# Optimization experiments

Hardware: AMD Instinct MI355X
Metric: run time of the kernel (lower is better)

## Reference

```python
import jax, jax.numpy as jnp
import numpy as np

N_NODES = 100000
N_EDGES = 1600000
N_FEAT = 128
N_HID = 128
N_CLASS = 10
N_GRAPHS = 512
BN_EPS = 1e-5


def setup_inputs() -> dict:
    key = jax.random.key(0)
    ks = jax.random.split(key, 12)
    x = jax.random.normal(ks[0], (N_NODES, N_FEAT), dtype=jnp.float32)
    edge_index = jax.random.randint(ks[1], (2, N_EDGES), 0, N_NODES, dtype=jnp.int32)
    batch = jnp.sort(jax.random.randint(ks[2], (N_NODES,), 0, N_GRAPHS, dtype=jnp.int32))
    s1 = 1.0 / np.sqrt(N_FEAT)
    s2 = 1.0 / np.sqrt(N_HID)
    W1 = jax.random.uniform(ks[3], (N_FEAT, N_HID), jnp.float32, -s1, s1)
    b1 = jax.random.uniform(ks[4], (N_HID,), jnp.float32, -s1, s1)
    gamma = jnp.ones((N_HID,), jnp.float32)
    beta = jnp.zeros((N_HID,), jnp.float32)
    W2 = jax.random.uniform(ks[5], (N_HID, N_HID), jnp.float32, -s2, s2)
    b2 = jax.random.uniform(ks[6], (N_HID,), jnp.float32, -s2, s2)
    clsW = jax.random.uniform(ks[7], (N_HID, N_CLASS), jnp.float32, -s2, s2)
    clsb = jax.random.uniform(ks[8], (N_CLASS,), jnp.float32, -s2, s2)
    return {"x": x, "edge_index": edge_index, "batch": batch,
            "W1": W1, "b1": b1, "gamma": gamma, "beta": beta,
            "W2": W2, "b2": b2, "clsW": clsW, "clsb": clsb}


def _gcn_norm(edge_index, n_nodes):
    # add self-loops, compute symmetric normalization D^-1/2 A_hat D^-1/2
    loops = jnp.arange(n_nodes, dtype=edge_index.dtype)
    src = jnp.concatenate([edge_index[0], loops])
    dst = jnp.concatenate([edge_index[1], loops])
    deg = jax.ops.segment_sum(jnp.ones_like(dst, dtype=jnp.float32), dst,
                              num_segments=n_nodes)
    dinv = jnp.where(deg > 0, jax.lax.rsqrt(deg), 0.0)
    norm = dinv[src] * dinv[dst]  # [E + N]
    return src, dst, norm


def _gcn_conv(h, src, dst, norm, W, b, n_nodes):
    h = h @ W                                   # [N, nhid] dense GEMM
    msg = h[src] * norm[:, None]                # gather + scale  [E+N, nhid]
    out = jax.ops.segment_sum(msg, dst, num_segments=n_nodes)  # scatter-add
    return out + b


def reference(x, edge_index, batch, W1, b1, gamma, beta, W2, b2, clsW, clsb):
    n_nodes = x.shape[0]
    src, dst, norm = _gcn_norm(edge_index, n_nodes)
    # layer 1: GCNConv -> BatchNorm(eval, running stats 0/1) -> ReLU -> Dropout(eval=id)
    h = _gcn_conv(x, src, dst, norm, W1, b1, n_nodes)
    h = h * (gamma / jnp.sqrt(1.0 + BN_EPS)) + beta
    h = jax.nn.relu(h)
    # layer 2: GCNConv (output layer, no bn/act)
    h = _gcn_conv(h, src, dst, norm, W2, b2, n_nodes)
    # global mean pool over batch index
    sums = jax.ops.segment_sum(h, batch, num_segments=N_GRAPHS)          # [G, nhid]
    cnts = jax.ops.segment_sum(jnp.ones((n_nodes,), h.dtype), batch,
                               num_segments=N_GRAPHS)
    g = sums / jnp.maximum(cnts, 1.0)[:, None]
    out = jax.nn.log_softmax(g @ clsW + clsb, axis=1)                    # [G, nclass]
    return out, g
```

## Files before the change

### kernel.cpp

```cpp
#include <hip/hip_runtime.h>
#include <hip/hip_bf16.h>

#define N_NODES 100000
#define N_EDGES 1600000
#define N_FEAT 128
#define N_HID 128
#define N_CLASS 10
#define N_GRAPHS 512
#define BN_RSQRT 0.9999950000374997f

#define NRANGE 12500
#define NSUB 512
#define SCAP 640
#define HGROUP 32
#define BPB (NSUB / HGROUP)

#define XT_STRIDE 136
#define YW_STRIDE 36
#define FG_LDS 78848

typedef _Float16 half_t;
typedef __attribute__((ext_vector_type(2))) _Float16 half2v;
typedef __attribute__((ext_vector_type(4))) _Float16 half4v;
typedef __attribute__((ext_vector_type(8))) _Float16 half8v;
typedef __attribute__((ext_vector_type(4))) float floatx4;
typedef __attribute__((ext_vector_type(2))) float floatx2;

__global__ __launch_bounds__(256) void bucket_fused(
    const int* __restrict__ src, const int* __restrict__ dst,
    int* __restrict__ cnt, unsigned long long* __restrict__ bucketed,
    const float* __restrict__ W1, half_t* __restrict__ Wt1,
    const float* __restrict__ W2, half_t* __restrict__ Wt2,
    const int* __restrict__ batch, int* __restrict__ boffs,
    int* __restrict__ sentinel,
    int chunkE, int E, int nnodes)
{
    __shared__ int wcnt[4][8];
    __shared__ int wbase[4][8];
    int blk = blockIdx.x;
    if (blk >= NSUB) {
        int k = blk - NSUB;
        if (k == 0) {
            if (threadIdx.x < 32) sentinel[threadIdx.x] = 0;
        } else if (k <= 128) {
            int i = (k - 1) * 256 + threadIdx.x;
            const float* W = (i < 16384) ? W1 : W2;
            half_t* Wt = (i < 16384) ? Wt1 : Wt2;
            int j = i & 16383;
            int c = j >> 7, kk = j & 127;
            Wt[(size_t)c * 128 + kk] = (half_t)W[(size_t)kk * 128 + c];
        } else {
            int i = (k - 129) * 256 + threadIdx.x;
            if (i < nnodes) {
                int b = batch[i];
                int prev = (i == 0) ? -1 : batch[i - 1];
                for (int g = prev + 1; g <= b; ++g) boffs[g] = i;
                if (i == nnodes - 1)
                    for (int g = b + 1; g <= N_GRAPHS; ++g) boffs[g] = nnodes;
            }
        }
        return;
    }
    int b = blk;
    int wave = threadIdx.x >> 6;
    int lane = threadIdx.x & 63;
    int e0 = b * chunkE;
    int e1 = e0 + chunkE < E ? e0 + chunkE : E;
    int iters = (chunkE + 255) / 256;

    int mycnt = 0;
    for (int it = 0; it < iters; ++it) {
        int e = e0 + it * 256 + threadIdx.x;
        bool valid = e < e1;
        int d = valid ? dst[e] : 0;
        int rr = (d * 8) / N_NODES;
#pragma unroll
        for (int r = 0; r < 8; ++r) {
            unsigned long long m = __ballot(valid && rr == r);
            if (lane == r) mycnt += __popcll(m);
        }
    }
    if (lane < 8) wcnt[wave][lane] = mycnt;
    __syncthreads();
    if (threadIdx.x < 8) {
        int r = threadIdx.x;
        int s = 0;
#pragma unroll
        for (int w = 0; w < 4; ++w) { wbase[w][r] = s; s += wcnt[w][r]; }
        cnt[r * NSUB + b] = s;
    }
    __syncthreads();

    int myoff = (lane < 8) ? wbase[wave][lane] : 0;
    for (int it = 0; it < iters; ++it) {
        int e = e0 + it * 256 + threadIdx.x;
        bool valid = e < e1;
        int s = valid ? src[e] : 0;
        int d = valid ? dst[e] : 0;
        int rr = (d * 8) / N_NODES;
        unsigned long long pk = ((unsigned long long)(unsigned)d << 32) | (unsigned)s;
#pragma unroll
        for (int r = 0; r < 8; ++r) {
            unsigned long long m = __ballot(valid && rr == r);
            int base_r = __shfl(myoff, r);
            if (valid && rr == r) {
                int pos = base_r + __popcll(m & ((1ull << lane) - 1));
                if (pos < SCAP)
                    bucketed[(size_t)(r * NSUB + b) * SCAP + pos] = pk;
            }
            if (lane == r) myoff += __popcll(m);
        }
    }
}

__global__ __launch_bounds__(256) void hist2(
    const unsigned long long* __restrict__ bucketed, const int* __restrict__ cnt,
    int* __restrict__ partial)
{
    __shared__ int h[NRANGE];
    int r = blockIdx.x & 7, g = blockIdx.x >> 3;
    for (int i = threadIdx.x; i < NRANGE; i += 256) h[i] = 0;
    __syncthreads();
    int rbase = r * NRANGE;
    for (int j = 0; j < BPB; ++j) {
        int b = g * BPB + j;
        int n = cnt[r * NSUB + b];
        if (n > SCAP) n = SCAP;
        const unsigned long long* seg = bucketed + (size_t)(r * NSUB + b) * SCAP;
        for (int i = threadIdx.x; i < n; i += 256)
            atomicAdd(&h[(int)(seg[i] >> 32) - rbase], 1);
    }
    __syncthreads();
    int* slice = partial + (size_t)(r * HGROUP + g) * NRANGE;
    for (int i = threadIdx.x; i < NRANGE; i += 256) slice[i] = h[i];
}

__global__ void deg_reduce(const int* __restrict__ partial, int* __restrict__ deg,
                           float* __restrict__ dinv, int* __restrict__ bsums, int n) {
    __shared__ int sm[256];
    int t = threadIdx.x;
    int i = blockIdx.x * 256 + t;
    int s = 0;
    if (i < n) {
        int rr = i / NRANGE;
        int dl = i - rr * NRANGE;
        const int* p = partial + (size_t)rr * HGROUP * NRANGE + dl;
#pragma unroll 8
        for (int g = 0; g < HGROUP; ++g) s += p[(size_t)g * NRANGE];
        deg[i] = s;
        dinv[i] = rsqrtf((float)s + 1.0f);
    }
    sm[t] = s;
    __syncthreads();
    for (int off = 128; off > 0; off >>= 1) {
        if (t < off) sm[t] += sm[t + off];
        __syncthreads();
    }
    if (t == 0) bsums[blockIdx.x] = sm[0];
}

__global__ void scan_small(int* __restrict__ bsums, int nb) {
    __shared__ int buf[1024];
    int t = threadIdx.x;
    int v = (t < nb) ? bsums[t] : 0;
    buf[t] = v;
    __syncthreads();
    for (int off = 1; off < 1024; off <<= 1) {
        int x = (t >= off) ? buf[t - off] : 0;
        __syncthreads();
        buf[t] += x;
        __syncthreads();
    }
    if (t < nb) bsums[t] = buf[t] - v;
}

__global__ __launch_bounds__(256) void scan_chunkoff(
    const int* __restrict__ in, const int* __restrict__ bsums,
    int* __restrict__ rowptr, int* __restrict__ partial, int n, int total)
{
    __shared__ int s[256];
    int t = threadIdx.x;
    int i = blockIdx.x * 256 + t;
    int v = (i < n) ? in[i] : 0;
    s[t] = v;
    __syncthreads();
    for (int off = 1; off < 256; off <<= 1) {
        int x = (t >= off) ? s[t - off] : 0;
        __syncthreads();
        s[t] += x;
        __syncthreads();
    }
    if (i == 0) rowptr[n] = total;
    if (i < n) {
        int excl = bsums[blockIdx.x] + s[t] - v;
        rowptr[i] = excl;
        int rr = i / NRANGE;
        int dl = i - rr * NRANGE;
        int* p = partial + (size_t)rr * HGROUP * NRANGE + dl;
        int vals[32];
#pragma unroll
        for (int g = 0; g < 32; ++g) vals[g] = p[(size_t)g * NRANGE];
        int running = excl;
#pragma unroll
        for (int g = 0; g < 32; ++g) {
            int tmp = vals[g];
            p[(size_t)g * NRANGE] = running;
            running += tmp;
        }
    }
}

__global__ __launch_bounds__(256, 2) void fill2_gemm1p(
    const unsigned long long* __restrict__ bucketed, const int* __restrict__ cnt,
    const int* __restrict__ partial, int* __restrict__ col,
    const float* __restrict__ X, const half_t* __restrict__ Wt,
    const float* __restrict__ dinv, unsigned char* __restrict__ Y8,
    int nrows, int ntiles)
{
    __shared__ __align__(16) unsigned char smem[FG_LDS];
    int tid = threadIdx.x;
    if (blockIdx.x < 256) {
        int* off = (int*)smem;
        int r = blockIdx.x & 7, g = blockIdx.x >> 3;
        const int* slice = partial + (size_t)(r * HGROUP + g) * NRANGE;
        for (int i = tid; i < NRANGE; i += 256) off[i] = slice[i];
        __syncthreads();
        int rbase = r * NRANGE;
        for (int j = 0; j < BPB; ++j) {
            int b = g * BPB + j;
            int n = cnt[r * NSUB + b];
            if (n > SCAP) n = SCAP;
            const unsigned long long* seg = bucketed + (size_t)(r * NSUB + b) * SCAP;
            for (int i = tid; i < n; i += 256) {
                unsigned long long pk = seg[i];
                int pos = atomicAdd(&off[(int)(pk >> 32) - rbase], 1);
                col[pos] = (int)((unsigned)(pk & 0xffffffffu) << 7);
            }
        }
        return;
    }
    half_t* wlds = (half_t*)smem;
    half_t* xb0  = (half_t*)(smem + 34816);
    half_t* xb1  = (half_t*)(smem + 52224);
    int* yw_all  = (int*)(smem + 69632);
    {
        const half8v* wg = (const half8v*)Wt;
        half8v w[8];
#pragma unroll
        for (int j = 0; j < 8; ++j) w[j] = wg[j * 256 + tid];
#pragma unroll
        for (int j = 0; j < 8; ++j) {
            int idx = j * 256 + tid;
            *(half8v*)(wlds + (idx >> 4) * XT_STRIDE + ((idx & 15) << 3)) = w[j];
        }
    }
    int wave = tid >> 6;
    int lane = tid & 63;
    int n16  = lane & 15;
    int quad = lane >> 4;
    int* yw = yw_all + wave * (16 * YW_STRIDE);
    int stride = gridDim.x - 256;

    int t = blockIdx.x - 256;
    if (t >= ntiles) return;
    half_t* xbc = xb0;
    half_t* xbn = xb1;
    {
        const float4* xg = (const float4*)(X + (size_t)t * 64 * 128);
        int idxmax = (nrows - t * 64) * 32;
#pragma unroll
        for (int j = 0; j < 8; ++j) {
            int idx = j * 256 + tid;
            if (idx < idxmax) {
                float4 f = xg[idx];
                half4v h = {(half_t)f.x, (half_t)f.y, (half_t)f.z, (half_t)f.w};
                *(half4v*)(xbc + (idx >> 5) * XT_STRIDE + ((idx & 31) << 2)) = h;
            }
        }
    }
    __syncthreads();
    for (;;) {
        int tn = t + stride;
        bool pf = tn < ntiles;
        float4 f[8];
        if (pf) {
            const float4* xg = (const float4*)(X + (size_t)tn * 64 * 128);
            int idxmax = (nrows - tn * 64) * 32;
#pragma unroll
            for (int j = 0; j < 8; ++j) {
                int idx = j * 256 + tid;
                f[j] = (idx < idxmax) ? xg[idx] : float4{0.f, 0.f, 0.f, 0.f};
            }
        }
        int r0 = t * 64 + wave * 16;
        bool active = r0 < nrows;
        int packedv[8];
        if (active) {
            const half_t* xr = xbc + (wave * 16 + n16) * XT_STRIDE;
            half8v a0 = *(const half8v*)(xr + 0 * 32 + quad * 8);
            half8v a1 = *(const half8v*)(xr + 1 * 32 + quad * 8);
            half8v a2 = *(const half8v*)(xr + 2 * 32 + quad * 8);
            half8v a3 = *(const half8v*)(xr + 3 * 32 + quad * 8);
            float dr = dinv[r0 + n16];
#pragma unroll
            for (int c = 0; c < 8; ++c) {
                const half_t* wl = wlds + (c * 16 + n16) * XT_STRIDE;
                floatx4 acc = {0.f, 0.f, 0.f, 0.f};
                acc = __builtin_amdgcn_mfma_f32_16x16x32_f16(*(const half8v*)(wl + 0 * 32 + quad * 8), a0, acc, 0, 0, 0);
                acc = __builtin_amdgcn_mfma_f32_16x16x32_f16(*(const half8v*)(wl + 1 * 32 + quad * 8), a1, acc, 0, 0, 0);
                acc = __builtin_amdgcn_mfma_f32_16x16x32_f16(*(const half8v*)(wl + 2 * 32 + quad * 8), a2, acc, 0, 0, 0);
                acc = __builtin_amdgcn_mfma_f32_16x16x32_f16(*(const half8v*)(wl + 3 * 32 + quad * 8), a3, acc, 0, 0, 0);
                int packed = __builtin_amdgcn_cvt_pk_fp8_f32(acc[0] * dr, acc[1] * dr, 0, false);
                packed = __builtin_amdgcn_cvt_pk_fp8_f32(acc[2] * dr, acc[3] * dr, packed, true);
                packedv[c] = packed;
            }
#pragma unroll
            for (int c = 0; c < 8; ++c)
                yw[n16 * YW_STRIDE + c * 4 + quad] = packedv[c];
#pragma unroll
            for (int u = 0; u < 2; ++u) {
                int4 v = *(const int4*)(yw + (u * 8 + (lane >> 3)) * YW_STRIDE + (lane & 7) * 4);
                *(int4*)(Y8 + (size_t)r0 * 128 + u * 1024 + lane * 16) = v;
            }
        }
        __syncthreads();
        if (!pf) break;
        {
            int idxmax = (nrows - tn * 64) * 32;
#pragma unroll
            for (int j = 0; j < 8; ++j) {
                int idx = j * 256 + tid;
                if (idx < idxmax) {
                    half4v h = {(half_t)f[j].x, (half_t)f[j].y, (half_t)f[j].z, (half_t)f[j].w};
                    *(half4v*)(xbn + (idx >> 5) * XT_STRIDE + ((idx & 31) << 2)) = h;
                }
            }
        }
        __syncthreads();
        half_t* tmp = xbc; xbc = xbn; xbn = tmp;
        t = tn;
    }
}

__global__ __launch_bounds__(256, 2) void gemm2_mfma(
    const half_t* __restrict__ X, const half_t* __restrict__ Wt,
    const float* __restrict__ dinv, unsigned char* __restrict__ Y8,
    int nrows, int ntiles)
{
    __shared__ __align__(16) half_t wlds[128 * XT_STRIDE];
    __shared__ __align__(16) half_t xb[2][64 * XT_STRIDE];
    __shared__ __align__(16) int yw_all[4 * 16 * YW_STRIDE];
    int tid = threadIdx.x;
    {
        const half8v* wg = (const half8v*)Wt;
        half8v w[8];
#pragma unroll
        for (int j = 0; j < 8; ++j) w[j] = wg[j * 256 + tid];
#pragma unroll
        for (int j = 0; j < 8; ++j) {
            int idx = j * 256 + tid;
            *(half8v*)(wlds + (idx >> 4) * XT_STRIDE + ((idx & 15) << 3)) = w[j];
        }
    }
    int wave = tid >> 6;
    int lane = tid & 63;
    int n16  = lane & 15;
    int quad = lane >> 4;
    int* yw = yw_all + wave * (16 * YW_STRIDE);

    int t = blockIdx.x;
    if (t >= ntiles) return;
    int cur = 0;
    {
        const half8v* xg = (const half8v*)(X + (size_t)t * 64 * 128);
        int idxmax = (nrows - t * 64) * 16;
#pragma unroll
        for (int j = 0; j < 4; ++j) {
            int idx = j * 256 + tid;
            if (idx < idxmax)
                *(half8v*)(xb[0] + (idx >> 4) * XT_STRIDE + ((idx & 15) << 3)) = xg[idx];
        }
    }
    __syncthreads();
    for (;;) {
        int tn = t + gridDim.x;
        bool pf = tn < ntiles;
        half8v v[4];
        if (pf) {
            const half8v* xg = (const half8v*)(X + (size_t)tn * 64 * 128);
            int idxmax = (nrows - tn * 64) * 16;
#pragma unroll
            for (int j = 0; j < 4; ++j) {
                int idx = j * 256 + tid;
                if (idx < idxmax) v[j] = xg[idx];
            }
        }
        int r0 = t * 64 + wave * 16;
        bool active = r0 < nrows;
        int packedv[8];
        if (active) {
            const half_t* xr = xb[cur] + (wave * 16 + n16) * XT_STRIDE;
            half8v a0 = *(const half8v*)(xr + 0 * 32 + quad * 8);
            half8v a1 = *(const half8v*)(xr + 1 * 32 + quad * 8);
            half8v a2 = *(const half8v*)(xr + 2 * 32 + quad * 8);
            half8v a3 = *(const half8v*)(xr + 3 * 32 + quad * 8);
            float dr = dinv[r0 + n16];
#pragma unroll
            for (int c = 0; c < 8; ++c) {
                const half_t* wl = wlds + (c * 16 + n16) * XT_STRIDE;
                floatx4 acc = {0.f, 0.f, 0.f, 0.f};
                acc = __builtin_amdgcn_mfma_f32_16x16x32_f16(*(const half8v*)(wl + 0 * 32 + quad * 8), a0, acc, 0, 0, 0);
                acc = __builtin_amdgcn_mfma_f32_16x16x32_f16(*(const half8v*)(wl + 1 * 32 + quad * 8), a1, acc, 0, 0, 0);
                acc = __builtin_amdgcn_mfma_f32_16x16x32_f16(*(const half8v*)(wl + 2 * 32 + quad * 8), a2, acc, 0, 0, 0);
                acc = __builtin_amdgcn_mfma_f32_16x16x32_f16(*(const half8v*)(wl + 3 * 32 + quad * 8), a3, acc, 0, 0, 0);
                int packed = __builtin_amdgcn_cvt_pk_fp8_f32(acc[0] * dr, acc[1] * dr, 0, false);
                packed = __builtin_amdgcn_cvt_pk_fp8_f32(acc[2] * dr, acc[3] * dr, packed, true);
                packedv[c] = packed;
            }
#pragma unroll
            for (int c = 0; c < 8; ++c)
                yw[n16 * YW_STRIDE + c * 4 + quad] = packedv[c];
#pragma unroll
            for (int u = 0; u < 2; ++u) {
                int4 o = *(const int4*)(yw + (u * 8 + (lane >> 3)) * YW_STRIDE + (lane & 7) * 4);
                *(int4*)(Y8 + (size_t)r0 * 128 + u * 1024 + lane * 16) = o;
            }
        }
        __syncthreads();
        if (!pf) break;
        {
            int idxmax = (nrows - tn * 64) * 16;
#pragma unroll
            for (int j = 0; j < 4; ++j) {
                int idx = j * 256 + tid;
                if (idx < idxmax)
                    *(half8v*)(xb[cur ^ 1] + (idx >> 4) * XT_STRIDE + ((idx & 15) << 3)) = v[j];
            }
        }
        __syncthreads();
        cur ^= 1;
        t = tn;
    }
}

__global__ __launch_bounds__(256, 4) void agg_fp8(
    const unsigned char* __restrict__ hs, half_t* __restrict__ out,
    const int* __restrict__ col, const int* __restrict__ rowptr,
    const float* __restrict__ bias,
    const float* __restrict__ gamma, const float* __restrict__ beta,
    int nnodes, int do_bn_relu)
{
    int wave = threadIdx.x >> 6;
    int lane = threadIdx.x & 63;
    int q16 = lane & 48;
    int l16 = lane & 15;
    int q = lane >> 4;
    int nb4 = (blockIdx.x * 4 + wave) * 4;
    int i = nb4 + q;
    bool valid = i < nnodes;
    unsigned iq = valid ? (unsigned)i : (unsigned)nnodes;
    unsigned f8 = (unsigned)l16 << 3;
    unsigned ZOFF = (unsigned)nnodes << 7;

    int e0 = valid ? rowptr[i] : 0;
    int e1 = valid ? rowptr[i + 1] : 0;
    int deg = e1 - e0;
    int m = deg;
    m = max(m, __shfl_xor(m, 16));
    m = max(m, __shfl_xor(m, 32));
    int nchunk = (m + 15) >> 4;

    unsigned long long us = *(const unsigned long long*)(hs + ((iq << 7) | f8));

    floatx2 a0 = {0.f, 0.f}, a1 = {0.f, 0.f}, a2 = {0.f, 0.f}, a3 = {0.f, 0.f};
    for (int t = 0; t < nchunk; ++t) {
        int idx = e0 + t * 16 + l16;
        unsigned cv = (idx < e1) ? (unsigned)col[idx] : ZOFF;
#pragma unroll
        for (int half = 0; half < 2; ++half) {
            const int kk = half * 8;
            unsigned long long v0, v1, v2, v3, v4, v5, v6, v7;
#define AGG_ADDR(K)                                                            \
            ({ unsigned rr = (unsigned)__shfl((int)cv, kk + K + q16);          \
               *(const unsigned long long*)(hs + (rr | f8)); })
            v0 = AGG_ADDR(0);
            v1 = AGG_ADDR(1);
            v2 = AGG_ADDR(2);
            v3 = AGG_ADDR(3);
            v4 = AGG_ADDR(4);
            v5 = AGG_ADDR(5);
            v6 = AGG_ADDR(6);
            v7 = AGG_ADDR(7);
#undef AGG_ADDR
#define AGG_ACC(V)                                                             \
            { unsigned lo = (unsigned)(V), hi = (unsigned)((V) >> 32);         \
              a0 += __builtin_amdgcn_cvt_pk_f32_fp8((int)lo, false);           \
              a1 += __builtin_amdgcn_cvt_pk_f32_fp8((int)lo, true);            \
              a2 += __builtin_amdgcn_cvt_pk_f32_fp8((int)hi, false);           \
              a3 += __builtin_amdgcn_cvt_pk_f32_fp8((int)hi, true); }
            AGG_ACC(v0) AGG_ACC(v1) AGG_ACC(v2) AGG_ACC(v3)
            AGG_ACC(v4) AGG_ACC(v5) AGG_ACC(v6) AGG_ACC(v7)
#undef AGG_ACC
        }
    }
    {
        unsigned lo = (unsigned)us, hi = (unsigned)(us >> 32);
        a0 += __builtin_amdgcn_cvt_pk_f32_fp8((int)lo, false);
        a1 += __builtin_amdgcn_cvt_pk_f32_fp8((int)lo, true);
        a2 += __builtin_amdgcn_cvt_pk_f32_fp8((int)hi, false);
        a3 += __builtin_amdgcn_cvt_pk_f32_fp8((int)hi, true);
    }

    if (!valid) return;
    float di = rsqrtf((float)deg + 1.0f);
    int fbase = l16 * 8;
    float4 bi0 = *(const float4*)(bias + fbase);
    float4 bi1 = *(const float4*)(bias + fbase + 4);
    float o0 = fmaf(di, a0.x, bi0.x);
    float o1 = fmaf(di, a0.y, bi0.y);
    float o2 = fmaf(di, a1.x, bi0.z);
    float o3 = fmaf(di, a1.y, bi0.w);
    float o4 = fmaf(di, a2.x, bi1.x);
    float o5 = fmaf(di, a2.y, bi1.y);
    float o6 = fmaf(di, a3.x, bi1.z);
    float o7 = fmaf(di, a3.y, bi1.w);
    if (do_bn_relu) {
        float4 ga0 = *(const float4*)(gamma + fbase);
        float4 ga1 = *(const float4*)(gamma + fbase + 4);
        float4 be0 = *(const float4*)(beta + fbase);
        float4 be1 = *(const float4*)(beta + fbase + 4);
        o0 = fmaf(o0, ga0.x * BN_RSQRT, be0.x);
        o1 = fmaf(o1, ga0.y * BN_RSQRT, be0.y);
        o2 = fmaf(o2, ga0.z * BN_RSQRT, be0.z);
        o3 = fmaf(o3, ga0.w * BN_RSQRT, be0.w);
        o4 = fmaf(o4, ga1.x * BN_RSQRT, be1.x);
        o5 = fmaf(o5, ga1.y * BN_RSQRT, be1.y);
        o6 = fmaf(o6, ga1.z * BN_RSQRT, be1.z);
        o7 = fmaf(o7, ga1.w * BN_RSQRT, be1.w);
        o0 = o0 > 0.f ? o0 : 0.f;
        o1 = o1 > 0.f ? o1 : 0.f;
        o2 = o2 > 0.f ? o2 : 0.f;
        o3 = o3 > 0.f ? o3 : 0.f;
        o4 = o4 > 0.f ? o4 : 0.f;
        o5 = o5 > 0.f ? o5 : 0.f;
        o6 = o6 > 0.f ? o6 : 0.f;
        o7 = o7 > 0.f ? o7 : 0.f;
    }
    half8v ov = {(half_t)o0, (half_t)o1, (half_t)o2, (half_t)o3,
                 (half_t)o4, (half_t)o5, (half_t)o6, (half_t)o7};
    *(half8v*)(out + (size_t)i * 128 + fbase) = ov;
}

__global__ __launch_bounds__(512) void pool_cls(
    const half_t* __restrict__ h, const int* __restrict__ boffs,
    const float* __restrict__ clsW, const float* __restrict__ clsb,
    float* __restrict__ gout, float* __restrict__ out)
{
    __shared__ float red[8][128];
    __shared__ float zbuf[16];
    int g = blockIdx.x;
    int w = threadIdx.x >> 6;
    int lane = threadIdx.x & 63;
    int n0 = boffs[g], n1 = boffs[g + 1];
    float ax = 0.f, ay = 0.f;
    for (int n = n0 + w; n < n1; n += 8) {
        half2v v = *(const half2v*)(h + (size_t)n * 128 + lane * 2);
        ax += (float)v.x;
        ay += (float)v.y;
    }
    red[w][lane * 2] = ax;
    red[w][lane * 2 + 1] = ay;
    __syncthreads();
    if (w == 0) {
        float sx = 0.f, sy = 0.f;
#pragma unroll
        for (int j = 0; j < 8; ++j) {
            sx += red[j][lane * 2];
            sy += red[j][lane * 2 + 1];
        }
        float cnt = (float)((n1 - n0) > 1 ? (n1 - n0) : 1);
        float g0 = sx / cnt, g1 = sy / cnt;
        gout[(size_t)g * 128 + lane * 2] = g0;
        gout[(size_t)g * 128 + lane * 2 + 1] = g1;
        red[0][lane * 2] = g0;
        red[0][lane * 2 + 1] = g1;
    }
    __syncthreads();
    if (threadIdx.x < N_CLASS) {
        int c = threadIdx.x;
        float z = clsb[c];
        for (int k = 0; k < N_HID; ++k)
            z = fmaf(red[0][k], clsW[k * N_CLASS + c], z);
        zbuf[c] = z;
    }
    __syncthreads();
    if (threadIdx.x == 0) {
        float m = zbuf[0];
#pragma unroll
        for (int c = 1; c < N_CLASS; ++c) m = fmaxf(m, zbuf[c]);
        float s = 0.f;
#pragma unroll
        for (int c = 0; c < N_CLASS; ++c) s += expf(zbuf[c] - m);
        float l = logf(s);
#pragma unroll
        for (int c = 0; c < N_CLASS; ++c)
            out[(size_t)g * N_CLASS + c] = zbuf[c] - m - l;
    }
}

extern "C" void kernel_launch(void* const* d_in, const int* in_sizes, int n_in,
                              void* d_out, int out_size, void* d_ws, size_t ws_size,
                              hipStream_t stream) {
    const float* x     = (const float*)d_in[0];
    const int*   ei    = (const int*)d_in[1];
    const int*   batch = (const int*)d_in[2];
    const float* W1    = (const float*)d_in[3];
    const float* b1    = (const float*)d_in[4];
    const float* gamma = (const float*)d_in[5];
    const float* beta  = (const float*)d_in[6];
    const float* W2    = (const float*)d_in[7];
    const float* b2    = (const float*)d_in[8];
    const float* clsW  = (const float*)d_in[9];
    const float* clsb  = (const float*)d_in[10];

    const int N = in_sizes[0] / N_FEAT;
    const int E = in_sizes[1] / 2;
    const int* src = ei;
    const int* dst = ei + E;

    unsigned char* BA8 = (unsigned char*)d_ws;
    half_t* BB = (half_t*)(BA8 + (size_t)(N + 1) * 128);
    half_t* Wt1 = BB + (size_t)N * 128;
    half_t* Wt2 = Wt1 + 16384;
    int*   col     = (int*)(Wt2 + 16384);
    int*   rowptr  = col + E;
    int*   deg     = rowptr + (N + 4);
    float* dinv    = (float*)(deg + N);
    int*   cnt     = (int*)(dinv + N);
    unsigned long long* bucketed =
        (unsigned long long*)(cnt + 8 * NSUB);
    int*   partial = (int*)(bucketed + (size_t)8 * NSUB * SCAP);
    int*   boffs   = partial + 8 * HGROUP * NRANGE;
    int*   bsums   = boffs + N_GRAPHS + 4;

    const int nb = (N + 255) / 256;
    const int chunkE = (E + NSUB - 1) / NSUB;
    const int ntiles = (N + 63) / 64;
    const int aggBlocks = (N + 15) / 16;

    bucket_fused<<<NSUB + 129 + nb, 256, 0, stream>>>(
        src, dst, cnt, bucketed, W1, Wt1, W2, Wt2, batch, boffs,
        (int*)(BA8 + (size_t)N * 128), chunkE, E, N);
    hist2<<<8 * HGROUP, 256, 0, stream>>>(bucketed, cnt, partial);
    deg_reduce<<<nb, 256, 0, stream>>>(partial, deg, dinv, bsums, N);
    scan_small<<<1, 1024, 0, stream>>>(bsums, nb);
    scan_chunkoff<<<nb, 256, 0, stream>>>(deg, bsums, rowptr, partial, N, E);
    fill2_gemm1p<<<256 + 512, 256, 0, stream>>>(
        bucketed, cnt, partial, col, x, Wt1, dinv, BA8, N, ntiles);
    agg_fp8<<<aggBlocks, 256, 0, stream>>>(BA8, BB, col, rowptr, b1, gamma, beta, N, 1);
    gemm2_mfma<<<512, 256, 0, stream>>>(BB, Wt2, dinv, BA8, N, ntiles);
    agg_fp8<<<aggBlocks, 256, 0, stream>>>(BA8, BB, col, rowptr, b2, gamma, beta, N, 0);

    float* out = (float*)d_out;
    float* gsec = out + (size_t)N_GRAPHS * N_CLASS;
    pool_cls<<<N_GRAPHS, 512, 0, stream>>>(BB, boffs, clsW, clsb, gsec, out);
}
```

Measured before the change: 281.9 us.

## Compute degree histogram in bucket kernel and fuse hist2 with degree reduce

Adds 64 extra blocks to the bucketing kernel that build a per-range degree histogram straight from the dst array, each scanning one eighth of the edges and keeping only the destinations that fall in its range. The degree reduction, which now sums 8 partials instead of 32, is merged into the same launch as the per-bucket histogram, removing one kernel launch and the serial dependency between them. In exchange, the dst array is read once more per range (eight full passes in total), and the bucketing kernel now reserves a large static LDS array for every block, including the bucketing blocks that never use it. That can lower occupancy for the main bucketing work.

```diff
diff --git a/kernel.cpp b/kernel.cpp
--- a/kernel.cpp
+++ b/kernel.cpp
@@ -14,6 +14,7 @@
 #define SCAP 640
 #define HGROUP 32
 #define BPB (NSUB / HGROUP)
+#define DGRP 8
 
 #define XT_STRIDE 136
 #define YW_STRIDE 36
@@ -29,28 +30,45 @@
 __global__ __launch_bounds__(256) void bucket_fused(
     const int* __restrict__ src, const int* __restrict__ dst,
     int* __restrict__ cnt, unsigned long long* __restrict__ bucketed,
+    int* __restrict__ dpartial,
     const float* __restrict__ W1, half_t* __restrict__ Wt1,
     const float* __restrict__ W2, half_t* __restrict__ Wt2,
     const int* __restrict__ batch, int* __restrict__ boffs,
     int* __restrict__ sentinel,
     int chunkE, int E, int nnodes)
 {
+    __shared__ int h[NRANGE];
     __shared__ int wcnt[4][8];
     __shared__ int wbase[4][8];
     int blk = blockIdx.x;
     if (blk >= NSUB) {
         int k = blk - NSUB;
-        if (k == 0) {
+        if (k < 64) {
+            int r = k & 7, g = k >> 3;
+            for (int i = threadIdx.x; i < NRANGE; i += 256) h[i] = 0;
+            __syncthreads();
+            int gb = (E + DGRP - 1) / DGRP;
+            int eb = g * gb;
+            int ee = eb + gb < E ? eb + gb : E;
+            int rbase = r * NRANGE;
+            for (int e = eb + threadIdx.x; e < ee; e += 256) {
+                unsigned rel = (unsigned)(dst[e] - rbase);
+                if (rel < NRANGE) atomicAdd(&h[rel], 1);
+            }
+            __syncthreads();
+            int* sl = dpartial + (size_t)(r * DGRP + g) * NRANGE;
+            for (int i = threadIdx.x; i < NRANGE; i += 256) sl[i] = h[i];
+        } else if (k == 64) {
             if (threadIdx.x < 32) sentinel[threadIdx.x] = 0;
-        } else if (k <= 128) {
-            int i = (k - 1) * 256 + threadIdx.x;
+        } else if (k <= 192) {
+            int i = (k - 65) * 256 + threadIdx.x;
             const float* W = (i < 16384) ? W1 : W2;
             half_t* Wt = (i < 16384) ? Wt1 : Wt2;
             int j = i & 16383;
             int c = j >> 7, kk = j & 127;
             Wt[(size_t)c * 128 + kk] = (half_t)W[(size_t)kk * 128 + c];
         } else {
-            int i = (k - 129) * 256 + threadIdx.x;
+            int i = (k - 193) * 256 + threadIdx.x;
             if (i < nnodes) {
                 int b = batch[i];
                 int prev = (i == 0) ? -1 : batch[i - 1];
@@ -113,40 +131,42 @@
     }
 }
 
-__global__ __launch_bounds__(256) void hist2(
+__global__ __launch_bounds__(256) void hist2_deg8(
     const unsigned long long* __restrict__ bucketed, const int* __restrict__ cnt,
-    int* __restrict__ partial)
+    int* __restrict__ partial,
+    const int* __restrict__ dpartial, int* __restrict__ deg,
+    float* __restrict__ dinv, int* __restrict__ bsums, int n)
 {
     __shared__ int h[NRANGE];
-    int r = blockIdx.x & 7, g = blockIdx.x >> 3;
-    for (int i = threadIdx.x; i < NRANGE; i += 256) h[i] = 0;
-    __syncthreads();
-    int rbase = r * NRANGE;
-    for (int j = 0; j < BPB; ++j) {
-        int b = g * BPB + j;
-        int n = cnt[r * NSUB + b];
-        if (n > SCAP) n = SCAP;
-        const unsigned long long* seg = bucketed + (size_t)(r * NSUB + b) * SCAP;
-        for (int i = threadIdx.x; i < n; i += 256)
-            atomicAdd(&h[(int)(seg[i] >> 32) - rbase], 1);
-    }
-    __syncthreads();
-    int* slice = partial + (size_t)(r * HGROUP + g) * NRANGE;
-    for (int i = threadIdx.x; i < NRANGE; i += 256) slice[i] = h[i];
-}
-
-__global__ void deg_reduce(const int* __restrict__ partial, int* __restrict__ deg,
-                           float* __restrict__ dinv, int* __restrict__ bsums, int n) {
     __shared__ int sm[256];
+    if (blockIdx.x < 256) {
+        int r = blockIdx.x & 7, g = blockIdx.x >> 3;
+        for (int i = threadIdx.x; i < NRANGE; i += 256) h[i] = 0;
+        __syncthreads();
+        int rbase = r * NRANGE;
+        for (int j = 0; j < BPB; ++j) {
+            int b = g * BPB + j;
+            int nn = cnt[r * NSUB + b];
+            if (nn > SCAP) nn = SCAP;
+            const unsigned long long* seg = bucketed + (size_t)(r * NSUB + b) * SCAP;
+            for (int i = threadIdx.x; i < nn; i += 256)
+                atomicAdd(&h[(int)(seg[i] >> 32) - rbase], 1);
+        }
+        __syncthreads();
+        int* slice = partial + (size_t)(r * HGROUP + g) * NRANGE;
+        for (int i = threadIdx.x; i < NRANGE; i += 256) slice[i] = h[i];
+        return;
+    }
+    int bi = blockIdx.x - 256;
     int t = threadIdx.x;
-    int i = blockIdx.x * 256 + t;
+    int i = bi * 256 + t;
     int s = 0;
     if (i < n) {
         int rr = i / NRANGE;
         int dl = i - rr * NRANGE;
-        const int* p = partial + (size_t)rr * HGROUP * NRANGE + dl;
-#pragma unroll 8
-        for (int g = 0; g < HGROUP; ++g) s += p[(size_t)g * NRANGE];
+        const int* p = dpartial + (size_t)(rr * DGRP) * NRANGE + dl;
+#pragma unroll
+        for (int g = 0; g < DGRP; ++g) s += p[(size_t)g * NRANGE];
         deg[i] = s;
         dinv[i] = rsqrtf((float)s + 1.0f);
     }
@@ -156,7 +176,7 @@
         if (t < off) sm[t] += sm[t + off];
         __syncthreads();
     }
-    if (t == 0) bsums[blockIdx.x] = sm[0];
+    if (t == 0) bsums[bi] = sm[0];
 }
 
 __global__ void scan_small(int* __restrict__ bsums, int nb) {
@@ -640,7 +660,8 @@
     unsigned long long* bucketed =
         (unsigned long long*)(cnt + 8 * NSUB);
     int*   partial = (int*)(bucketed + (size_t)8 * NSUB * SCAP);
-    int*   boffs   = partial + 8 * HGROUP * NRANGE;
+    int*   dpartial = partial + 8 * HGROUP * NRANGE;
+    int*   boffs   = dpartial + 8 * DGRP * NRANGE;
     int*   bsums   = boffs + N_GRAPHS + 4;
 
     const int nb = (N + 255) / 256;
@@ -648,11 +669,11 @@
     const int ntiles = (N + 63) / 64;
     const int aggBlocks = (N + 15) / 16;
 
-    bucket_fused<<<NSUB + 129 + nb, 256, 0, stream>>>(
-        src, dst, cnt, bucketed, W1, Wt1, W2, Wt2, batch, boffs,
+    bucket_fused<<<NSUB + 64 + 129 + nb, 256, 0, stream>>>(
+        src, dst, cnt, bucketed, dpartial, W1, Wt1, W2, Wt2, batch, boffs,
         (int*)(BA8 + (size_t)N * 128), chunkE, E, N);
-    hist2<<<8 * HGROUP, 256, 0, stream>>>(bucketed, cnt, partial);
-    deg_reduce<<<nb, 256, 0, stream>>>(partial, deg, dinv, bsums, N);
+    hist2_deg8<<<256 + nb, 256, 0, stream>>>(
+        bucketed, cnt, partial, dpartial, deg, dinv, bsums, N);
     scan_small<<<1, 1024, 0, stream>>>(bsums, nb);
     scan_chunkoff<<<nb, 256, 0, stream>>>(deg, bsums, rowptr, partial, N, E);
     fill2_gemm1p<<<256 + 512, 256, 0, stream>>>(
```

Result: slower. 493.3 us (+75.0%).
